# Kernel tuning notes

Hardware: AMD Instinct MI355X
Metric: run time of the kernel (lower is better)

## Reference

```python
import jax, jax.numpy as jnp
import numpy as np

B, L, NE, DOUT = 4, 4096, 64, 64
DI = 128          # backbone model dim (hardcoded d_inner in MambaDoc)
NL = 2            # num_layers
H = 2             # num_heads
N = 128           # state_dim
G = 1             # num_groups
CONV = 4          # conv_size
DIN = 2 * DI      # expand=2 -> 256 inner channels of the mixer
P = DIN // H      # headdim = 128
CCH = DIN + 2 * G * N      # 512 conv channels (x, B, C)
DPROJ = 2 * DIN + 2 * G * N + H  # 770 in_proj output width


def setup_inputs() -> dict:
    key = jax.random.key(0)
    ks = jax.random.split(key, 8)
    s = lambda k, shape, sc: (jax.random.normal(k, shape, jnp.float32) * sc)
    return {
        "x": s(ks[0], (B, L, NE), 1.0),
        "in_w": s(ks[1], (DI, NE), (1.0 / NE) ** 0.5),
        "in_b": jnp.zeros((DI,), jnp.float32),
        "out_w": s(ks[2], (DOUT, DI), (1.0 / DI) ** 0.5),
        "out_b": jnp.zeros((DOUT,), jnp.float32),
        "l_rms_w": jnp.ones((NL, DI), jnp.float32),
        "l_in_w": s(ks[3], (NL, DPROJ, DI), (1.0 / DI) ** 0.5),
        "conv_w": s(ks[4], (NL, CCH, CONV), (1.0 / CONV) ** 0.5),
        "conv_b": jnp.zeros((NL, CCH), jnp.float32),
        "dt_bias": s(ks[5], (NL, H), 0.1),
        "A_log": jnp.zeros((NL, H), jnp.float32),   # A = -exp(A_log) = -1
        "D_p": jnp.ones((NL, H), jnp.float32),
        "gnorm_w": jnp.ones((NL, DIN), jnp.float32),
        "l_out_w": s(ks[6], (NL, DI, DIN), (1.0 / DIN) ** 0.5),
        "fnorm_w": jnp.ones((DI,), jnp.float32),
    }


def _rms(x, w, eps=1e-5):
    return x * jax.lax.rsqrt(jnp.mean(x * x, -1, keepdims=True) + eps) * w


def _mamba_layer(x, rms_w, in_w, cw, cb, dtb, a_log, d, gnw, ow):
    # x: (B,L,DI)
    h = _rms(x, rms_w)
    zxbcdt = jnp.einsum("bld,ed->ble", h, in_w)  # (B,L,770)
    z, xBC, dt = jnp.split(zxbcdt, [DIN, DIN + CCH], axis=-1)
    # causal depthwise conv over time, conv_size taps
    xp = jnp.pad(xBC, ((0, 0), (CONV - 1, 0), (0, 0)))
    xc = cb + sum(xp[:, k:k + L, :] * cw[:, k] for k in range(CONV))
    xc = jax.nn.silu(xc)
    xs, Bm, Cm = jnp.split(xc, [DIN, DIN + G * N], axis=-1)
    xs = xs.reshape(B, L, H, P)
    dt = jax.nn.softplus(dt + dtb)                 # (B,L,H)
    dA = jnp.exp(dt * (-jnp.exp(a_log)))           # (B,L,H) discrete decay

    def step(hc, inp):
        dA_t, dt_t, x_t, B_t, C_t = inp  # (B,H),(B,H),(B,H,P),(B,N),(B,N)
        hc = hc * dA_t[:, :, None, None] + (dt_t[:, :, None] * x_t)[..., None] * B_t[:, None, None, :]
        y = jnp.einsum("bhpn,bn->bhp", hc, C_t)
        return hc, y

    h0 = jnp.zeros((B, H, P, N), x.dtype)
    seq = (jnp.moveaxis(dA, 1, 0), jnp.moveaxis(dt, 1, 0), jnp.moveaxis(xs, 1, 0),
           jnp.moveaxis(Bm, 1, 0), jnp.moveaxis(Cm, 1, 0))
    _, ys = jax.lax.scan(step, h0, seq)
    y = jnp.moveaxis(ys, 0, 1)                     # (B,L,H,P)
    y = y + xs * d[None, None, :, None]            # D skip connection
    y = _rms(y.reshape(B, L, DIN) * jax.nn.silu(z), gnw)  # gated RMSNorm
    return x + jnp.einsum("ble,de->bld", y, ow)


def reference(x, in_w, in_b, out_w, out_b, l_rms_w, l_in_w, conv_w, conv_b,
              dt_bias, A_log, D_p, gnorm_w, l_out_w, fnorm_w):
    xp = jnp.einsum("bln,dn->bld", x, in_w) + in_b
    h = xp
    for i in range(NL):
        h = _mamba_layer(h, l_rms_w[i], l_in_w[i], conv_w[i], conv_b[i],
                         dt_bias[i], A_log[i], D_p[i], gnorm_w[i], l_out_w[i])
    h = _rms(h, fnorm_w)            # backbone final norm
    out = xp + h                    # outer residual in MambaDoc.forward
    return jnp.einsum("bld,od->blo", out, out_w) + out_b
```

## Files before the change

kernel.cpp:

```cpp
#include <hip/hip_runtime.h>
#include <cstddef>
#include <cstdint>


#define LSEQ 4096
#define MTOK 16384

typedef unsigned short u16;
typedef _Float16 f16x8 __attribute__((ext_vector_type(8)));
typedef float f32x4 __attribute__((ext_vector_type(4)));

__device__ __forceinline__ u16 f2h(float x) {
    return __builtin_bit_cast(u16, (_Float16)x);
}
__device__ __forceinline__ float h2f(u16 u) {
    return (float)__builtin_bit_cast(_Float16, u);
}
__device__ __forceinline__ float silu_f(float x) { return x / (1.f + __expf(-x)); }

__device__ __forceinline__ void async_lds16(const void* g, void* l) {
    __builtin_amdgcn_global_load_lds(
        (const __attribute__((address_space(1))) unsigned int*)g,
        (__attribute__((address_space(3))) unsigned int*)l, 16, 0, 0);
}

__device__ __forceinline__ uint4 cvt8(const float* __restrict__ src) {
    float4 a = *(const float4*)src;
    float4 b = *(const float4*)(src + 4);
    union { u16 u[8]; uint4 q; } pk;
    pk.u[0] = f2h(a.x); pk.u[1] = f2h(a.y); pk.u[2] = f2h(a.z); pk.u[3] = f2h(a.w);
    pk.u[4] = f2h(b.x); pk.u[5] = f2h(b.y); pk.u[6] = f2h(b.z); pk.u[7] = f2h(b.w);
    return pk.q;
}

__device__ __forceinline__ uint4 cvt8g(const float* __restrict__ src,
                                       const float* __restrict__ gw) {
    float4 a = *(const float4*)src;
    float4 b = *(const float4*)(src + 4);
    float4 ga = *(const float4*)gw;
    float4 gb = *(const float4*)(gw + 4);
    union { u16 u[8]; uint4 q; } pk;
    pk.u[0] = f2h(a.x * ga.x); pk.u[1] = f2h(a.y * ga.y);
    pk.u[2] = f2h(a.z * ga.z); pk.u[3] = f2h(a.w * ga.w);
    pk.u[4] = f2h(b.x * gb.x); pk.u[5] = f2h(b.y * gb.y);
    pk.u[6] = f2h(b.z * gb.z); pk.u[7] = f2h(b.w * gb.w);
    return pk.q;
}

__global__ __launch_bounds__(256) void gemm_rms0_kernel(
    const float* __restrict__ xf, const float* __restrict__ wf,
    const float* __restrict__ bias, const float* __restrict__ rmsw,
    u16* __restrict__ xp16, u16* __restrict__ hbuf16, u16* __restrict__ hn16)
{
    __shared__ u16 sA[64 * 64];
    __shared__ u16 sW[128 * 64];
    __shared__ float red[64][33];
    __shared__ float srstd[64];
    const int m0 = blockIdx.y * 64;
    const int tid = threadIdx.x, wid = tid >> 6, lane = tid & 63;
    const int wm = (wid >> 1) * 32, wn = (wid & 1) * 64;
    const int quad = lane >> 4, cl = lane & 15;
    #pragma unroll
    for (int i = 0; i < 2; i++) {
        int ck = i * 256 + tid;
        int r = ck >> 3, cc = ck & 7;
        int csw = (cc ^ (r & 7)) << 3;
        *(uint4*)&sA[ck * 8] = cvt8(xf + (size_t)(m0 + r) * 64 + csw);
    }
    #pragma unroll
    for (int i = 0; i < 4; i++) {
        int ck = i * 256 + tid;
        int r = ck >> 3, cc = ck & 7;
        int csw = (cc ^ (r & 7)) << 3;
        *(uint4*)&sW[ck * 8] = cvt8(wf + (size_t)r * 64 + csw);
    }
    __syncthreads();
    f32x4 acc[2][4];
    #pragma unroll
    for (int i = 0; i < 2; i++)
        #pragma unroll
        for (int j = 0; j < 4; j++) acc[i][j] = f32x4{0.f, 0.f, 0.f, 0.f};
    #pragma unroll
    for (int ks = 0; ks < 2; ks++) {
        f16x8 af[2], wv[4];
        int kc = ks * 4 + quad;
        #pragma unroll
        for (int i = 0; i < 2; i++) {
            int r = wm + i * 16 + cl;
            af[i] = *(const f16x8*)&sA[r * 64 + ((kc ^ (r & 7)) << 3)];
        }
        #pragma unroll
        for (int j = 0; j < 4; j++) {
            int r = wn + j * 16 + cl;
            wv[j] = *(const f16x8*)&sW[r * 64 + ((kc ^ (r & 7)) << 3)];
        }
        #pragma unroll
        for (int i = 0; i < 2; i++)
            #pragma unroll
            for (int j = 0; j < 4; j++)
                acc[i][j] = __builtin_amdgcn_mfma_f32_16x16x32_f16(
                    af[i], wv[j], acc[i][j], 0, 0, 0);
    }
    const int slot = (wid & 1) * 16 + cl;
    #pragma unroll
    for (int i = 0; i < 2; i++)
        #pragma unroll
        for (int r = 0; r < 4; r++) {
            int t = wm + i * 16 + quad * 4 + r;
            float ssp = 0.f;
            #pragma unroll
            for (int j = 0; j < 4; j++) {
                int n = wn + j * 16 + cl;
                float v = acc[i][j][r] + bias[n];
                acc[i][j][r] = v;
                ssp += v * v;
            }
            red[t][slot] = ssp;
        }
    __syncthreads();
    if (tid < 64) {
        float s = 0.f;
        #pragma unroll
        for (int sl = 0; sl < 32; sl++) s += red[tid][sl];
        srstd[tid] = rsqrtf(s * (1.f / 128.f) + 1e-5f);
    }
    __syncthreads();
    #pragma unroll
    for (int i = 0; i < 2; i++)
        #pragma unroll
        for (int r = 0; r < 4; r++) {
            int t = wm + i * 16 + quad * 4 + r;
            size_t ob = (size_t)(m0 + t) * 128;
            float rstd = srstd[t];
            #pragma unroll
            for (int j = 0; j < 4; j++) {
                int n = wn + j * 16 + cl;
                float v = acc[i][j][r];
                u16 vh = f2h(v);
                xp16[ob + n] = vh;
                hbuf16[ob + n] = vh;
                hn16[ob + n] = f2h(v * rstd * rmsw[n]);
            }
        }
}

__global__ __launch_bounds__(256) void gemm_inproj_kernel(
    const u16* __restrict__ A, const float* __restrict__ Wf,
    u16* __restrict__ zx16, float* __restrict__ dtb, float* __restrict__ Sb,
    const float* __restrict__ dt_bias, const float* __restrict__ A_log)
{
    __shared__ u16 sA[128 * 64];
    __shared__ u16 sW[128 * 64];
    __shared__ float sdt[2][128];
    const int K = 128, N = 770;
    const int n0 = blockIdx.x * 128, m0 = blockIdx.y * 128;
    const int tid = threadIdx.x, wid = tid >> 6, lane = tid & 63;
    const int wm = (wid >> 1) * 64, wn = (wid & 1) * 64;
    const int quad = lane >> 4, cl = lane & 15;
    f32x4 acc[4][4];
    #pragma unroll
    for (int i = 0; i < 4; i++)
        #pragma unroll
        for (int j = 0; j < 4; j++) acc[i][j] = f32x4{0.f, 0.f, 0.f, 0.f};

    for (int k0 = 0; k0 < K; k0 += 64) {
        #pragma unroll
        for (int i = 0; i < 4; i++) {
            int ck = i * 256 + tid;
            int r = ck >> 3, cc = ck & 7;
            int csw = (cc ^ (r & 7)) << 3;
            async_lds16(A + (size_t)(m0 + r) * K + k0 + csw,
                        (void*)(sA + (i * 256 + (tid & ~63)) * 8));
        }
        #pragma unroll
        for (int i = 0; i < 4; i++) {
            int ck = i * 256 + tid;
            int r = ck >> 3, cc = ck & 7;
            int csw = (cc ^ (r & 7)) << 3;
            int rr = n0 + r; if (rr >= N) rr = N - 1;
            *(uint4*)&sW[ck * 8] = cvt8(Wf + (size_t)rr * K + k0 + csw);
        }
        __syncthreads();
        #pragma unroll
        for (int ks = 0; ks < 2; ks++) {
            f16x8 af[4], wv[4];
            int kc = ks * 4 + quad;
            #pragma unroll
            for (int i = 0; i < 4; i++) {
                int r = wm + i * 16 + cl;
                af[i] = *(const f16x8*)&sA[r * 64 + ((kc ^ (r & 7)) << 3)];
            }
            #pragma unroll
            for (int j = 0; j < 4; j++) {
                int r = wn + j * 16 + cl;
                wv[j] = *(const f16x8*)&sW[r * 64 + ((kc ^ (r & 7)) << 3)];
            }
            #pragma unroll
            for (int i = 0; i < 4; i++)
                #pragma unroll
                for (int j = 0; j < 4; j++)
                    acc[i][j] = __builtin_amdgcn_mfma_f32_16x16x32_f16(
                        af[i], wv[j], acc[i][j], 0, 0, 0);
        }
        __syncthreads();
    }
    if (blockIdx.x < 6) {
        #pragma unroll
        for (int i = 0; i < 4; i++) {
            int m = m0 + wm + i * 16 + quad * 4;
            #pragma unroll
            for (int j = 0; j < 4; j++) {
                int n = n0 + wn + j * 16 + cl;
                #pragma unroll
                for (int r = 0; r < 4; r++)
                    zx16[(size_t)(m + r) * 768 + n] = f2h(acc[i][j][r]);
            }
        }
    } else {
        if ((wid & 1) == 0 && cl < 2) {
            #pragma unroll
            for (int i = 0; i < 4; i++)
                #pragma unroll
                for (int r = 0; r < 4; r++)
                    sdt[cl][wm + i * 16 + quad * 4 + r] = acc[i][0][r];
        }
        __syncthreads();
        const int hh = tid >> 7, t = tid & 127;
        float raw = sdt[hh][t] + dt_bias[hh];
        float dt = fmaxf(raw, 0.f) + log1pf(__expf(-fabsf(raw)));
        dtb[(size_t)(m0 + t) * 2 + hh] = dt;
        float ad = -__expf(A_log[hh]) * dt;
        __syncthreads();
        sdt[hh][t] = ad;
        __syncthreads();
        for (int off = 1; off < 128; off <<= 1) {
            float add = (t >= off) ? sdt[hh][t - off] : 0.f;
            __syncthreads();
            sdt[hh][t] += add;
            __syncthreads();
        }
        Sb[(size_t)(m0 + t) * 2 + hh] = sdt[hh][t];
    }
}

__global__ __launch_bounds__(512) void chunkstate_conv_kernel(
    const u16* __restrict__ zx16, const float* __restrict__ cw,
    const float* __restrict__ cb, const float* __restrict__ dtb,
    const float* __restrict__ Sb, u16* __restrict__ Hb)
{
    __shared__ u16 raw[2560 * 8];
    __shared__ u16 XT[128 * 128];
    __shared__ u16 BT[128 * 128];
    __shared__ float scw[2][128][4];
    __shared__ float scb[2][128];
    __shared__ float ssw[128];
    const int c = blockIdx.x, h = blockIdx.y, b = blockIdx.z;
    const int tid = threadIdx.x, wid = tid >> 6, lane = tid & 63;
    const int quad = lane >> 4, cl = lane & 15;
    const int tok0 = b * LSEQ + c * 128;
    for (int idx = tid; idx < 256; idx += 512) {
        int grp = idx >> 7, j = idx & 127;
        int ch = grp ? (256 + j) : (128 * h + j);
        float4 w4 = *(const float4*)&cw[ch * 4];
        scw[grp][j][0] = w4.x; scw[grp][j][1] = w4.y;
        scw[grp][j][2] = w4.z; scw[grp][j][3] = w4.w;
        scb[grp][j] = cb[ch];
    }
    if (tid < 128) {
        float Sl = Sb[(size_t)(tok0 + 127) * 2 + h];
        ssw[tid] = __expf(Sl - Sb[(size_t)(tok0 + tid) * 2 + h])
                   * dtb[(size_t)(tok0 + tid) * 2 + h];
    }
    #pragma unroll
    for (int i = 0; i < 5; i++) {
        int ck = i * 512 + tid;
        int r = ck >> 4; if (r > 130) r = 130;
        int cc = ck & 15;
        int tok = tok0 - 3 + r; if (tok < 0) tok = 0;
        async_lds16(zx16 + (size_t)tok * 768 + 256 + 128 * h + ((cc ^ (r & 15)) << 3),
                    (void*)(raw + (i * 512 + (tid & ~63)) * 8));
    }
    __syncthreads();
    if (c == 0 && tid < 48) *(uint4*)&raw[tid * 8] = make_uint4(0, 0, 0, 0);
    __syncthreads();
    #pragma unroll
    for (int it = 0; it < 4; it++) {
        int idx = it * 512 + tid;
        int s = idx & 127, pg = idx >> 7;
        f16x8 v[4];
        #pragma unroll
        for (int k = 0; k < 4; k++) {
            int rr = s + k;
            v[k] = *(const f16x8*)&raw[rr * 128 + ((pg ^ (rr & 15)) << 3)];
        }
        #pragma unroll
        for (int j = 0; j < 8; j++) {
            int p = pg * 8 + j;
            float o = scb[0][p] + (float)v[0][j] * scw[0][p][0]
                    + (float)v[1][j] * scw[0][p][1]
                    + (float)v[2][j] * scw[0][p][2]
                    + (float)v[3][j] * scw[0][p][3];
            o = silu_f(o);
            XT[p * 128 + (((s >> 3) ^ (p & 15)) << 3) + (s & 7)] = f2h(o);
        }
    }
    __syncthreads();
    #pragma unroll
    for (int i = 0; i < 5; i++) {
        int ck = i * 512 + tid;
        int r = ck >> 4; if (r > 130) r = 130;
        int cc = ck & 15;
        int tok = tok0 - 3 + r; if (tok < 0) tok = 0;
        async_lds16(zx16 + (size_t)tok * 768 + 512 + ((cc ^ (r & 15)) << 3),
                    (void*)(raw + (i * 512 + (tid & ~63)) * 8));
    }
    __syncthreads();
    if (c == 0 && tid < 48) *(uint4*)&raw[tid * 8] = make_uint4(0, 0, 0, 0);
    __syncthreads();
    #pragma unroll
    for (int it = 0; it < 4; it++) {
        int idx = it * 512 + tid;
        int s = idx & 127, ng = idx >> 7;
        f16x8 v[4];
        #pragma unroll
        for (int k = 0; k < 4; k++) {
            int rr = s + k;
            v[k] = *(const f16x8*)&raw[rr * 128 + ((ng ^ (rr & 15)) << 3)];
        }
        float wsv = ssw[s];
        #pragma unroll
        for (int j = 0; j < 8; j++) {
            int n = ng * 8 + j;
            float o = scb[1][n] + (float)v[0][j] * scw[1][n][0]
                    + (float)v[1][j] * scw[1][n][1]
                    + (float)v[2][j] * scw[1][n][2]
                    + (float)v[3][j] * scw[1][n][3];
            o = silu_f(o) * wsv;
            BT[n * 128 + (((s >> 3) ^ (n & 15)) << 3) + (s & 7)] = f2h(o);
        }
    }
    __syncthreads();
    const size_t blk = ((size_t)((b * 2 + h) * 32 + c)) << 14;
    const int wm = (wid >> 1) * 32, wn = (wid & 1) * 64;
    f32x4 acc[2][4];
    #pragma unroll
    for (int i = 0; i < 2; i++)
        #pragma unroll
        for (int j = 0; j < 4; j++) acc[i][j] = f32x4{0.f, 0.f, 0.f, 0.f};
    #pragma unroll
    for (int ks = 0; ks < 4; ks++) {
        f16x8 xa[2], bb[4];
        int kc = ks * 4 + quad;
        #pragma unroll
        for (int i = 0; i < 2; i++) {
            int r = wm + i * 16 + cl;
            xa[i] = *(const f16x8*)&XT[r * 128 + ((kc ^ (r & 15)) << 3)];
        }
        #pragma unroll
        for (int j = 0; j < 4; j++) {
            int r = wn + j * 16 + cl;
            bb[j] = *(const f16x8*)&BT[r * 128 + ((kc ^ (r & 15)) << 3)];
        }
        #pragma unroll
        for (int i = 0; i < 2; i++)
            #pragma unroll
            for (int j = 0; j < 4; j++)
                acc[i][j] = __builtin_amdgcn_mfma_f32_16x16x32_f16(
                    xa[i], bb[j], acc[i][j], 0, 0, 0);
    }
    u16* out = Hb + blk;
    #pragma unroll
    for (int i = 0; i < 2; i++)
        #pragma unroll
        for (int j = 0; j < 4; j++)
            #pragma unroll
            for (int r = 0; r < 4; r++)
                out[(size_t)(wm + i * 16 + quad * 4 + r) * 128 + wn + j * 16 + cl]
                    = f2h(acc[i][j][r]);
}

__global__ __launch_bounds__(256) void statecombine_kernel(
    const float* __restrict__ Sb, const u16* __restrict__ Hb,
    u16* __restrict__ Hbf)
{
    const int e = blockIdx.x * 256 + threadIdx.x;
    const int h = blockIdx.y, b = blockIdx.z;
    const size_t base = ((size_t)((b * 2 + h) * 32)) << 14;
    float state = 0.f;
    for (int c = 0; c < 32; c++) {
        size_t idx = base + ((size_t)c << 14) + e;
        float v = h2f(Hb[idx]);
        Hbf[idx] = f2h(state);
        float dec = __expf(Sb[(size_t)(b * LSEQ + c * 128 + 127) * 2 + h]);
        state = dec * state + v;
    }
}

__global__ __launch_bounds__(512) void ssd_ph_kernel(
    const u16* __restrict__ zx16, const u16* __restrict__ Hbf,
    const float* __restrict__ dtb, const float* __restrict__ Sb,
    const float* __restrict__ cw, const float* __restrict__ cb,
    const float* __restrict__ Dp, u16* __restrict__ g16)
{
    __shared__ u16 raw[2560 * 8];
    __shared__ u16 XT[128 * 128];
    __shared__ u16 Btok[128 * 128];
    __shared__ u16 Ctok[128 * 128];
    __shared__ float sS[128], sdt[128];
    __shared__ float scw[3][128][4];
    __shared__ float scb[3][128];
    const int c = blockIdx.x, h = blockIdx.y, b = blockIdx.z;
    const int tid = threadIdx.x, wid = tid >> 6, lane = tid & 63;
    const int quad = lane >> 4, cl = lane & 15;
    const int tok0 = b * LSEQ + c * 128;
    const size_t blk = ((size_t)((b * 2 + h) * 32 + c)) << 14;
    for (int idx = tid; idx < 384; idx += 512) {
        int grp = idx >> 7, j = idx & 127;
        int ch = (grp == 0) ? (128 * h + j) : (grp == 1 ? 256 + j : 384 + j);
        float4 w4 = *(const float4*)&cw[ch * 4];
        scw[grp][j][0] = w4.x; scw[grp][j][1] = w4.y;
        scw[grp][j][2] = w4.z; scw[grp][j][3] = w4.w;
        scb[grp][j] = cb[ch];
    }
    if (tid < 128) {
        sS[tid] = Sb[(size_t)(tok0 + tid) * 2 + h];
        sdt[tid] = dtb[(size_t)(tok0 + tid) * 2 + h];
    }
    #pragma unroll
    for (int i = 0; i < 5; i++) {
        int ck = i * 512 + tid;
        int r = ck >> 4; if (r > 130) r = 130;
        int cc = ck & 15;
        int tok = tok0 - 3 + r; if (tok < 0) tok = 0;
        async_lds16(zx16 + (size_t)tok * 768 + 256 + 128 * h + ((cc ^ (r & 15)) << 3),
                    (void*)(raw + (i * 512 + (tid & ~63)) * 8));
    }
    __syncthreads();
    if (c == 0 && tid < 48) *(uint4*)&raw[tid * 8] = make_uint4(0, 0, 0, 0);
    __syncthreads();
    #pragma unroll
    for (int it = 0; it < 4; it++) {
        int idx = it * 512 + tid;
        int s = idx & 127, pg = idx >> 7;
        f16x8 v[4];
        #pragma unroll
        for (int k = 0; k < 4; k++) {
            int rr = s + k;
            v[k] = *(const f16x8*)&raw[rr * 128 + ((pg ^ (rr & 15)) << 3)];
        }
        #pragma unroll
        for (int j = 0; j < 8; j++) {
            int p = pg * 8 + j;
            float o = scb[0][p] + (float)v[0][j] * scw[0][p][0]
                    + (float)v[1][j] * scw[0][p][1]
                    + (float)v[2][j] * scw[0][p][2]
                    + (float)v[3][j] * scw[0][p][3];
            XT[p * 128 + (((s >> 3) ^ (p & 15)) << 3) + (s & 7)] = f2h(silu_f(o));
        }
    }
    __syncthreads();
    #pragma unroll
    for (int i = 0; i < 5; i++) {
        int ck = i * 512 + tid;
        int r = ck >> 4; if (r > 130) r = 130;
        int cc = ck & 15;
        int tok = tok0 - 3 + r; if (tok < 0) tok = 0;
        async_lds16(zx16 + (size_t)tok * 768 + 512 + ((cc ^ (r & 15)) << 3),
                    (void*)(raw + (i * 512 + (tid & ~63)) * 8));
    }
    __syncthreads();
    if (c == 0 && tid < 48) *(uint4*)&raw[tid * 8] = make_uint4(0, 0, 0, 0);
    __syncthreads();
    #pragma unroll
    for (int it = 0; it < 4; it++) {
        int idx = it * 512 + tid;
        int t = idx & 127, ng = idx >> 7;
        f16x8 v[4];
        #pragma unroll
        for (int k = 0; k < 4; k++) {
            int rr = t + k;
            v[k] = *(const f16x8*)&raw[rr * 128 + ((ng ^ (rr & 15)) << 3)];
        }
        union { u16 u[8]; uint4 q; } pk;
        #pragma unroll
        for (int j = 0; j < 8; j++) {
            int n = ng * 8 + j;
            float o = scb[1][n] + (float)v[0][j] * scw[1][n][0]
                    + (float)v[1][j] * scw[1][n][1]
                    + (float)v[2][j] * scw[1][n][2]
                    + (float)v[3][j] * scw[1][n][3];
            pk.u[j] = f2h(silu_f(o));
        }
        *(uint4*)&Btok[t * 128 + ((ng ^ (t & 15)) << 3)] = pk.q;
    }
    __syncthreads();
    #pragma unroll
    for (int i = 0; i < 5; i++) {
        int ck = i * 512 + tid;
        int r = ck >> 4; if (r > 130) r = 130;
        int cc = ck & 15;
        int tok = tok0 - 3 + r; if (tok < 0) tok = 0;
        async_lds16(zx16 + (size_t)tok * 768 + 640 + ((cc ^ (r & 15)) << 3),
                    (void*)(raw + (i * 512 + (tid & ~63)) * 8));
    }
    __syncthreads();
    if (c == 0 && tid < 48) *(uint4*)&raw[tid * 8] = make_uint4(0, 0, 0, 0);
    __syncthreads();
    #pragma unroll
    for (int it = 0; it < 4; it++) {
        int idx = it * 512 + tid;
        int t = idx & 127, ng = idx >> 7;
        f16x8 v[4];
        #pragma unroll
        for (int k = 0; k < 4; k++) {
            int rr = t + k;
            v[k] = *(const f16x8*)&raw[rr * 128 + ((ng ^ (rr & 15)) << 3)];
        }
        union { u16 u[8]; uint4 q; } pk;
        #pragma unroll
        for (int j = 0; j < 8; j++) {
            int n = ng * 8 + j;
            float o = scb[2][n] + (float)v[0][j] * scw[2][n][0]
                    + (float)v[1][j] * scw[2][n][1]
                    + (float)v[2][j] * scw[2][n][2]
                    + (float)v[3][j] * scw[2][n][3];
            pk.u[j] = f2h(silu_f(o));
        }
        *(uint4*)&Ctok[t * 128 + ((ng ^ (t & 15)) << 3)] = pk.q;
    }
    __syncthreads();
    #pragma unroll
    for (int i = 0; i < 4; i++) {
        int ck = i * 512 + tid;
        int r = ck >> 4, cc = ck & 15;
        async_lds16(Hbf + blk + (size_t)r * 128 + ((cc ^ (r & 15)) << 3),
                    (void*)(raw + (i * 512 + (tid & ~63)) * 8));
    }
    __syncthreads();
    const int wm = (wid >> 1) * 32, wn = (wid & 1) * 64;
    f32x4 acc[2][4];
    #pragma unroll
    for (int i = 0; i < 2; i++)
        #pragma unroll
        for (int j = 0; j < 4; j++) acc[i][j] = f32x4{0.f, 0.f, 0.f, 0.f};
    #pragma unroll
    for (int ks = 0; ks < 4; ks++) {
        f16x8 ca[2], hb[4];
        int kc = ks * 4 + quad;
        #pragma unroll
        for (int i = 0; i < 2; i++) {
            int r = wm + i * 16 + cl;
            ca[i] = *(const f16x8*)&Ctok[r * 128 + ((kc ^ (r & 15)) << 3)];
        }
        #pragma unroll
        for (int j = 0; j < 4; j++) {
            int r = wn + j * 16 + cl;
            hb[j] = *(const f16x8*)&raw[r * 128 + ((kc ^ (r & 15)) << 3)];
        }
        #pragma unroll
        for (int i = 0; i < 2; i++)
            #pragma unroll
            for (int j = 0; j < 4; j++)
                acc[i][j] = __builtin_amdgcn_mfma_f32_16x16x32_f16(
                    ca[i], hb[j], acc[i][j], 0, 0, 0);
    }
    #pragma unroll
    for (int i = 0; i < 2; i++)
        #pragma unroll
        for (int r = 0; r < 4; r++) {
            float e = __expf(sS[wm + i * 16 + quad * 4 + r]);
            #pragma unroll
            for (int j = 0; j < 4; j++) acc[i][j][r] *= e;
        }
    f32x4 sacc[2][4];
    #pragma unroll
    for (int i = 0; i < 2; i++)
        #pragma unroll
        for (int j = 0; j < 4; j++) sacc[i][j] = f32x4{0.f, 0.f, 0.f, 0.f};
    #pragma unroll
    for (int ks = 0; ks < 4; ks++) {
        f16x8 cs[2], bs[4];
        int kc = ks * 4 + quad;
        #pragma unroll
        for (int i2 = 0; i2 < 2; i2++) {
            int r = wm + i2 * 16 + cl;
            cs[i2] = *(const f16x8*)&Ctok[r * 128 + ((kc ^ (r & 15)) << 3)];
        }
        #pragma unroll
        for (int j = 0; j < 4; j++) {
            int r = wn + j * 16 + cl;
            bs[j] = *(const f16x8*)&Btok[r * 128 + ((kc ^ (r & 15)) << 3)];
        }
        #pragma unroll
        for (int i2 = 0; i2 < 2; i2++)
            #pragma unroll
            for (int j = 0; j < 4; j++)
                if (wm + i2 * 16 + 15 >= wn + j * 16)
                    sacc[i2][j] = __builtin_amdgcn_mfma_f32_16x16x32_f16(
                        cs[i2], bs[j], sacc[i2][j], 0, 0, 0);
    }
    __syncthreads();
    #pragma unroll
    for (int i2 = 0; i2 < 2; i2++)
        #pragma unroll
        for (int r = 0; r < 4; r++) {
            int t = wm + i2 * 16 + quad * 4 + r;
            float Stv = sS[t];
            #pragma unroll
            for (int j = 0; j < 4; j++) {
                int s = wn + j * 16 + cl;
                float gv = 0.f;
                if (s <= t) gv = sacc[i2][j][r] * __expf(Stv - sS[s]) * sdt[s];
                raw[t * 128 + (((s >> 3) ^ (t & 15)) << 3) + (s & 7)] = f2h(gv);
            }
        }
    __syncthreads();
    #pragma unroll
    for (int ks = 0; ks < 4; ks++) {
        f16x8 ga[2], xb[4];
        int kc = ks * 4 + quad;
        #pragma unroll
        for (int i = 0; i < 2; i++) {
            int r = wm + i * 16 + cl;
            ga[i] = *(const f16x8*)&raw[r * 128 + ((kc ^ (r & 15)) << 3)];
        }
        #pragma unroll
        for (int j = 0; j < 4; j++) {
            int r = wn + j * 16 + cl;
            xb[j] = *(const f16x8*)&XT[r * 128 + ((kc ^ (r & 15)) << 3)];
        }
        #pragma unroll
        for (int i = 0; i < 2; i++)
            #pragma unroll
            for (int j = 0; j < 4; j++)
                acc[i][j] = __builtin_amdgcn_mfma_f32_16x16x32_f16(
                    ga[i], xb[j], acc[i][j], 0, 0, 0);
    }
    const float dco = Dp[h];
    #pragma unroll
    for (int i = 0; i < 2; i++)
        #pragma unroll
        for (int r = 0; r < 4; r++) {
            int t = wm + i * 16 + quad * 4 + r;
            u16* row = g16 + (size_t)(tok0 + t) * 256 + h * 128;
            #pragma unroll
            for (int j = 0; j < 4; j++) {
                int p = wn + j * 16 + cl;
                float xv = h2f(XT[p * 128 + (((t >> 3) ^ (p & 15)) << 3) + (t & 7)]);
                float zv = h2f(zx16[(size_t)(tok0 + t) * 768 + h * 128 + p]);
                row[p] = f2h((acc[i][j][r] + dco * xv) * silu_f(zv));
            }
        }
}

__global__ __launch_bounds__(256) void gemm_outrms_kernel(
    const u16* __restrict__ A, const float* __restrict__ Wf,
    const float* __restrict__ gnw, const float* __restrict__ rmsw,
    u16* __restrict__ xp16, u16* __restrict__ hbuf16, u16* __restrict__ hn16,
    const float* __restrict__ out_wf, const float* __restrict__ out_b,
    float* __restrict__ dout, int mode)
{
    __shared__ u16 sA[64 * 64];
    __shared__ u16 sW[128 * 64];
    __shared__ float red[64][33];
    __shared__ float srstd[64];
    __shared__ float redp[64][5];
    __shared__ float rstdg[64];
    __shared__ u16 hn2[64 * 128];
    __shared__ u16 ow[64 * 128];
    const int K = 256;
    const int m0 = blockIdx.y * 64;
    const int tid = threadIdx.x, wid = tid >> 6, lane = tid & 63;
    const int wm = (wid >> 1) * 32, wn = (wid & 1) * 64;
    const int quad = lane >> 4, cl = lane & 15;
    {
        int t = tid >> 2, q = tid & 3;
        const u16* row = A + (size_t)(m0 + t) * 256 + q * 64;
        float ss = 0.f;
        #pragma unroll
        for (int u = 0; u < 8; u++) {
            f16x8 v = *(const f16x8*)&row[u * 8];
            #pragma unroll
            for (int j = 0; j < 8; j++) { float f = (float)v[j]; ss += f * f; }
        }
        redp[t][q] = ss;
    }
    __syncthreads();
    if (tid < 64)
        rstdg[tid] = rsqrtf((redp[tid][0] + redp[tid][1] + redp[tid][2]
                             + redp[tid][3]) * (1.f / 256.f) + 1e-5f);
    f32x4 acc[2][4];
    #pragma unroll
    for (int i = 0; i < 2; i++)
        #pragma unroll
        for (int j = 0; j < 4; j++) acc[i][j] = f32x4{0.f, 0.f, 0.f, 0.f};

    for (int k0 = 0; k0 < K; k0 += 64) {
        #pragma unroll
        for (int i = 0; i < 2; i++) {
            int ck = i * 256 + tid;
            int r = ck >> 3, cc = ck & 7;
            int csw = (cc ^ (r & 7)) << 3;
            async_lds16(A + (size_t)(m0 + r) * K + k0 + csw,
                        (void*)(sA + (i * 256 + (tid & ~63)) * 8));
        }
        #pragma unroll
        for (int i = 0; i < 4; i++) {
            int ck = i * 256 + tid;
            int r = ck >> 3, cc = ck & 7;
            int csw = (cc ^ (r & 7)) << 3;
            *(uint4*)&sW[ck * 8] = cvt8g(Wf + (size_t)r * K + k0 + csw,
                                         gnw + k0 + csw);
        }
        __syncthreads();
        #pragma unroll
        for (int ks = 0; ks < 2; ks++) {
            f16x8 af[2], wv[4];
            int kc = ks * 4 + quad;
            #pragma unroll
            for (int i = 0; i < 2; i++) {
                int r = wm + i * 16 + cl;
                af[i] = *(const f16x8*)&sA[r * 64 + ((kc ^ (r & 7)) << 3)];
            }
            #pragma unroll
            for (int j = 0; j < 4; j++) {
                int r = wn + j * 16 + cl;
                wv[j] = *(const f16x8*)&sW[r * 64 + ((kc ^ (r & 7)) << 3)];
            }
            #pragma unroll
            for (int i = 0; i < 2; i++)
                #pragma unroll
                for (int j = 0; j < 4; j++)
                    acc[i][j] = __builtin_amdgcn_mfma_f32_16x16x32_f16(
                        af[i], wv[j], acc[i][j], 0, 0, 0);
        }
        __syncthreads();
    }
    const int slot = (wid & 1) * 16 + cl;
    #pragma unroll
    for (int i = 0; i < 2; i++)
        #pragma unroll
        for (int r = 0; r < 4; r++) {
            int t = wm + i * 16 + quad * 4 + r;
            size_t ob = (size_t)(m0 + t) * 128;
            float rg = rstdg[t];
            float ssp = 0.f;
            #pragma unroll
            for (int j = 0; j < 4; j++) {
                int n = wn + j * 16 + cl;
                float v = acc[i][j][r] * rg + h2f(hbuf16[ob + n]);
                acc[i][j][r] = v;
                ssp += v * v;
            }
            red[t][slot] = ssp;
        }
    __syncthreads();
    if (tid < 64) {
        float s = 0.f;
        #pragma unroll
        for (int sl = 0; sl < 32; sl++) s += red[tid][sl];
        srstd[tid] = rsqrtf(s * (1.f / 128.f) + 1e-5f);
    }
    __syncthreads();
    #pragma unroll
    for (int i = 0; i < 2; i++)
        #pragma unroll
        for (int r = 0; r < 4; r++) {
            int t = wm + i * 16 + quad * 4 + r;
            size_t ob = (size_t)(m0 + t) * 128;
            float rstd = srstd[t];
            #pragma unroll
            for (int j = 0; j < 4; j++) {
                int n = wn + j * 16 + cl;
                float v = acc[i][j][r];
                float val = v * rstd * rmsw[n];
                if (mode == 1) {
                    hbuf16[ob + n] = f2h(v);
                    hn16[ob + n] = f2h(val);
                } else {
                    val += h2f(xp16[ob + n]);
                    hn2[t * 128 + (((n >> 3) ^ (t & 15)) << 3) + (n & 7)] = f2h(val);
                }
            }
        }
    if (mode == 1) return;
    #pragma unroll
    for (int i = 0; i < 4; i++) {
        int ck = i * 256 + tid;
        int rr = ck >> 4, cc = ck & 15;
        int csw = (cc ^ (rr & 15)) << 3;
        *(uint4*)&ow[ck * 8] = cvt8(out_wf + (size_t)rr * 128 + csw);
    }
    __syncthreads();
    const int wm4 = (wid >> 1) * 32, wn4 = (wid & 1) * 32;
    f32x4 acc2[2][2];
    #pragma unroll
    for (int i = 0; i < 2; i++)
        #pragma unroll
        for (int j = 0; j < 2; j++) acc2[i][j] = f32x4{0.f, 0.f, 0.f, 0.f};
    #pragma unroll
    for (int ks = 0; ks < 4; ks++) {
        f16x8 af2[2], wf2[2];
        int kc = ks * 4 + quad;
        #pragma unroll
        for (int i = 0; i < 2; i++) {
            int r = wm4 + i * 16 + cl;
            af2[i] = *(const f16x8*)&hn2[r * 128 + ((kc ^ (r & 15)) << 3)];
        }
        #pragma unroll
        for (int j = 0; j < 2; j++) {
            int rr = wn4 + j * 16 + cl;
            wf2[j] = *(const f16x8*)&ow[rr * 128 + ((kc ^ (rr & 15)) << 3)];
        }
        #pragma unroll
        for (int i = 0; i < 2; i++)
            #pragma unroll
            for (int j = 0; j < 2; j++)
                acc2[i][j] = __builtin_amdgcn_mfma_f32_16x16x32_f16(
                    af2[i], wf2[j], acc2[i][j], 0, 0, 0);
    }
    #pragma unroll
    for (int i = 0; i < 2; i++) {
        int m = m0 + wm4 + i * 16 + quad * 4;
        #pragma unroll
        for (int j = 0; j < 2; j++) {
            int n = wn4 + j * 16 + cl;
            float bv = out_b[n];
            #pragma unroll
            for (int r = 0; r < 4; r++)
                dout[(size_t)(m + r) * 64 + n] = acc2[i][j][r] + bv;
        }
    }
}

extern "C" void kernel_launch(void* const* d_in, const int* in_sizes, int n_in,
                              void* d_out, int out_size, void* d_ws, size_t ws_size,
                              hipStream_t stream)
{
    (void)in_sizes; (void)n_in; (void)out_size; (void)ws_size;
    const float* x       = (const float*)d_in[0];
    const float* in_w    = (const float*)d_in[1];
    const float* in_b    = (const float*)d_in[2];
    const float* out_w   = (const float*)d_in[3];
    const float* out_b   = (const float*)d_in[4];
    const float* l_rms_w = (const float*)d_in[5];
    const float* l_in_w  = (const float*)d_in[6];
    const float* conv_w  = (const float*)d_in[7];
    const float* conv_b  = (const float*)d_in[8];
    const float* dt_bias = (const float*)d_in[9];
    const float* A_log   = (const float*)d_in[10];
    const float* D_p     = (const float*)d_in[11];
    const float* gnorm_w = (const float*)d_in[12];
    const float* l_out_w = (const float*)d_in[13];
    const float* fnorm_w = (const float*)d_in[14];

    char* w = (char*)d_ws;
    u16*   xp16   = (u16*)(w);
    u16*   hbuf16 = (u16*)(w + 4194304);
    u16*   hn16   = (u16*)(w + 8388608);
    u16*   zx16   = (u16*)(w + 12582912);
    float* dtb    = (float*)(w + 37748736);
    float* Sb     = (float*)(w + 37879808);
    u16*   Hb     = (u16*)(w + 38010880);
    u16*   Hbf    = (u16*)(w + 46399488);
    u16*   g16    = (u16*)(w + 54788096);

    gemm_rms0_kernel<<<dim3(1, 256), 256, 0, stream>>>(
        x, in_w, in_b, l_rms_w, xp16, hbuf16, hn16);

    for (int i = 0; i < 2; i++) {
        gemm_inproj_kernel<<<dim3(7, 128), 256, 0, stream>>>(
            hn16, l_in_w + (size_t)i * 770 * 128, zx16, dtb, Sb,
            dt_bias + i * 2, A_log + i * 2);
        chunkstate_conv_kernel<<<dim3(32, 2, 4), 512, 0, stream>>>(
            zx16, conv_w + i * 2048, conv_b + i * 512, dtb, Sb, Hb);
        statecombine_kernel<<<dim3(64, 2, 4), 256, 0, stream>>>(Sb, Hb, Hbf);
        ssd_ph_kernel<<<dim3(32, 2, 4), 512, 0, stream>>>(
            zx16, Hbf, dtb, Sb, conv_w + i * 2048, conv_b + i * 512,
            D_p + i * 2, g16);
        gemm_outrms_kernel<<<dim3(1, 256), 256, 0, stream>>>(
            g16, l_out_w + (size_t)i * 128 * 256, gnorm_w + i * 256,
            (i == 0) ? (l_rms_w + 128) : fnorm_w, xp16, hbuf16, hn16,
            out_w, out_b, (float*)d_out, (i == 0) ? 1 : 3);
    }
}
```

Baseline: 231.4 us.

## Fuse chunk-state, state-combine and SSD kernels into one persistent kernel with grid barriers

Merges the three per-layer SSD kernels into a single 256-block kernel. Blocks sync through atomic-counter grid barriers between computing chunk states, scanning them across chunks, and producing outputs. The conv/silu of x and B is now computed once instead of being repeated in two kernels, and two launches per layer go away. The cost is spin-wait barriers, which assume all 256 blocks are co-resident (512 threads and large LDS per block), plus a memset of the counters.

```diff
diff --git a/kernel.cpp b/kernel.cpp
--- a/kernel.cpp
+++ b/kernel.cpp
@@ -45,6 +45,18 @@
     pk.u[4] = f2h(b.x * gb.x); pk.u[5] = f2h(b.y * gb.y);
     pk.u[6] = f2h(b.z * gb.z); pk.u[7] = f2h(b.w * gb.w);
     return pk.q;
+}
+
+__device__ __forceinline__ void grid_barrier(unsigned int* cnt, unsigned int target) {
+    __syncthreads();
+    if (threadIdx.x == 0) {
+        __threadfence();
+        atomicAdd(cnt, 1u);
+        while (atomicAdd(cnt, 0u) < target)
+            __builtin_amdgcn_s_sleep(8);
+        __threadfence();
+    }
+    __syncthreads();
 }
 
 __global__ __launch_bounds__(256) void gemm_rms0_kernel(
@@ -243,170 +255,18 @@
     }
 }
 
-__global__ __launch_bounds__(512) void chunkstate_conv_kernel(
-    const u16* __restrict__ zx16, const float* __restrict__ cw,
-    const float* __restrict__ cb, const float* __restrict__ dtb,
-    const float* __restrict__ Sb, u16* __restrict__ Hb)
+__global__ __launch_bounds__(512) void layer_ssd_kernel(
+    const u16* __restrict__ zx16, const float* __restrict__ dtb,
+    const float* __restrict__ Sb, const float* __restrict__ cw,
+    const float* __restrict__ cb, const float* __restrict__ Dp,
+    u16* __restrict__ Hb, u16* __restrict__ Hbf, u16* __restrict__ g16,
+    unsigned int* __restrict__ cnt)
 {
     __shared__ u16 raw[2560 * 8];
     __shared__ u16 XT[128 * 128];
-    __shared__ u16 BT[128 * 128];
-    __shared__ float scw[2][128][4];
-    __shared__ float scb[2][128];
-    __shared__ float ssw[128];
-    const int c = blockIdx.x, h = blockIdx.y, b = blockIdx.z;
-    const int tid = threadIdx.x, wid = tid >> 6, lane = tid & 63;
-    const int quad = lane >> 4, cl = lane & 15;
-    const int tok0 = b * LSEQ + c * 128;
-    for (int idx = tid; idx < 256; idx += 512) {
-        int grp = idx >> 7, j = idx & 127;
-        int ch = grp ? (256 + j) : (128 * h + j);
-        float4 w4 = *(const float4*)&cw[ch * 4];
-        scw[grp][j][0] = w4.x; scw[grp][j][1] = w4.y;
-        scw[grp][j][2] = w4.z; scw[grp][j][3] = w4.w;
-        scb[grp][j] = cb[ch];
-    }
-    if (tid < 128) {
-        float Sl = Sb[(size_t)(tok0 + 127) * 2 + h];
-        ssw[tid] = __expf(Sl - Sb[(size_t)(tok0 + tid) * 2 + h])
-                   * dtb[(size_t)(tok0 + tid) * 2 + h];
-    }
-    #pragma unroll
-    for (int i = 0; i < 5; i++) {
-        int ck = i * 512 + tid;
-        int r = ck >> 4; if (r > 130) r = 130;
-        int cc = ck & 15;
-        int tok = tok0 - 3 + r; if (tok < 0) tok = 0;
-        async_lds16(zx16 + (size_t)tok * 768 + 256 + 128 * h + ((cc ^ (r & 15)) << 3),
-                    (void*)(raw + (i * 512 + (tid & ~63)) * 8));
-    }
-    __syncthreads();
-    if (c == 0 && tid < 48) *(uint4*)&raw[tid * 8] = make_uint4(0, 0, 0, 0);
-    __syncthreads();
-    #pragma unroll
-    for (int it = 0; it < 4; it++) {
-        int idx = it * 512 + tid;
-        int s = idx & 127, pg = idx >> 7;
-        f16x8 v[4];
-        #pragma unroll
-        for (int k = 0; k < 4; k++) {
-            int rr = s + k;
-            v[k] = *(const f16x8*)&raw[rr * 128 + ((pg ^ (rr & 15)) << 3)];
-        }
-        #pragma unroll
-        for (int j = 0; j < 8; j++) {
-            int p = pg * 8 + j;
-            float o = scb[0][p] + (float)v[0][j] * scw[0][p][0]
-                    + (float)v[1][j] * scw[0][p][1]
-                    + (float)v[2][j] * scw[0][p][2]
-                    + (float)v[3][j] * scw[0][p][3];
-            o = silu_f(o);
-            XT[p * 128 + (((s >> 3) ^ (p & 15)) << 3) + (s & 7)] = f2h(o);
-        }
-    }
-    __syncthreads();
-    #pragma unroll
-    for (int i = 0; i < 5; i++) {
-        int ck = i * 512 + tid;
-        int r = ck >> 4; if (r > 130) r = 130;
-        int cc = ck & 15;
-        int tok = tok0 - 3 + r; if (tok < 0) tok = 0;
-        async_lds16(zx16 + (size_t)tok * 768 + 512 + ((cc ^ (r & 15)) << 3),
-                    (void*)(raw + (i * 512 + (tid & ~63)) * 8));
-    }
-    __syncthreads();
-    if (c == 0 && tid < 48) *(uint4*)&raw[tid * 8] = make_uint4(0, 0, 0, 0);
-    __syncthreads();
-    #pragma unroll
-    for (int it = 0; it < 4; it++) {
-        int idx = it * 512 + tid;
-        int s = idx & 127, ng = idx >> 7;
-        f16x8 v[4];
-        #pragma unroll
-        for (int k = 0; k < 4; k++) {
-            int rr = s + k;
-            v[k] = *(const f16x8*)&raw[rr * 128 + ((ng ^ (rr & 15)) << 3)];
-        }
-        float wsv = ssw[s];
-        #pragma unroll
-        for (int j = 0; j < 8; j++) {
-            int n = ng * 8 + j;
-            float o = scb[1][n] + (float)v[0][j] * scw[1][n][0]
-                    + (float)v[1][j] * scw[1][n][1]
-                    + (float)v[2][j] * scw[1][n][2]
-                    + (float)v[3][j] * scw[1][n][3];
-            o = silu_f(o) * wsv;
-            BT[n * 128 + (((s >> 3) ^ (n & 15)) << 3) + (s & 7)] = f2h(o);
-        }
-    }
-    __syncthreads();
-    const size_t blk = ((size_t)((b * 2 + h) * 32 + c)) << 14;
-    const int wm = (wid >> 1) * 32, wn = (wid & 1) * 64;
-    f32x4 acc[2][4];
-    #pragma unroll
-    for (int i = 0; i < 2; i++)
-        #pragma unroll
-        for (int j = 0; j < 4; j++) acc[i][j] = f32x4{0.f, 0.f, 0.f, 0.f};
-    #pragma unroll
-    for (int ks = 0; ks < 4; ks++) {
-        f16x8 xa[2], bb[4];
-        int kc = ks * 4 + quad;
-        #pragma unroll
-        for (int i = 0; i < 2; i++) {
-            int r = wm + i * 16 + cl;
-            xa[i] = *(const f16x8*)&XT[r * 128 + ((kc ^ (r & 15)) << 3)];
-        }
-        #pragma unroll
-        for (int j = 0; j < 4; j++) {
-            int r = wn + j * 16 + cl;
-            bb[j] = *(const f16x8*)&BT[r * 128 + ((kc ^ (r & 15)) << 3)];
-        }
-        #pragma unroll
-        for (int i = 0; i < 2; i++)
-            #pragma unroll
-            for (int j = 0; j < 4; j++)
-                acc[i][j] = __builtin_amdgcn_mfma_f32_16x16x32_f16(
-                    xa[i], bb[j], acc[i][j], 0, 0, 0);
-    }
-    u16* out = Hb + blk;
-    #pragma unroll
-    for (int i = 0; i < 2; i++)
-        #pragma unroll
-        for (int j = 0; j < 4; j++)
-            #pragma unroll
-            for (int r = 0; r < 4; r++)
-                out[(size_t)(wm + i * 16 + quad * 4 + r) * 128 + wn + j * 16 + cl]
-                    = f2h(acc[i][j][r]);
-}
-
-__global__ __launch_bounds__(256) void statecombine_kernel(
-    const float* __restrict__ Sb, const u16* __restrict__ Hb,
-    u16* __restrict__ Hbf)
-{
-    const int e = blockIdx.x * 256 + threadIdx.x;
-    const int h = blockIdx.y, b = blockIdx.z;
-    const size_t base = ((size_t)((b * 2 + h) * 32)) << 14;
-    float state = 0.f;
-    for (int c = 0; c < 32; c++) {
-        size_t idx = base + ((size_t)c << 14) + e;
-        float v = h2f(Hb[idx]);
-        Hbf[idx] = f2h(state);
-        float dec = __expf(Sb[(size_t)(b * LSEQ + c * 128 + 127) * 2 + h]);
-        state = dec * state + v;
-    }
-}
-
-__global__ __launch_bounds__(512) void ssd_ph_kernel(
-    const u16* __restrict__ zx16, const u16* __restrict__ Hbf,
-    const float* __restrict__ dtb, const float* __restrict__ Sb,
-    const float* __restrict__ cw, const float* __restrict__ cb,
-    const float* __restrict__ Dp, u16* __restrict__ g16)
-{
-    __shared__ u16 raw[2560 * 8];
-    __shared__ u16 XT[128 * 128];
+    __shared__ u16 slotA[128 * 128];
     __shared__ u16 Btok[128 * 128];
-    __shared__ u16 Ctok[128 * 128];
-    __shared__ float sS[128], sdt[128];
+    __shared__ float sS[128], sdt[128], ssw[128];
     __shared__ float scw[3][128][4];
     __shared__ float scb[3][128];
     const int c = blockIdx.x, h = blockIdx.y, b = blockIdx.z;
@@ -423,8 +283,12 @@
         scb[grp][j] = cb[ch];
     }
     if (tid < 128) {
-        sS[tid] = Sb[(size_t)(tok0 + tid) * 2 + h];
-        sdt[tid] = dtb[(size_t)(tok0 + tid) * 2 + h];
+        float Sv = Sb[(size_t)(tok0 + tid) * 2 + h];
+        float dv = dtb[(size_t)(tok0 + tid) * 2 + h];
+        sS[tid] = Sv;
+        sdt[tid] = dv;
+        float Sl = Sb[(size_t)(tok0 + 127) * 2 + h];
+        ssw[tid] = __expf(Sl - Sv) * dv;
     }
     #pragma unroll
     for (int i = 0; i < 5; i++) {
@@ -474,13 +338,14 @@
     #pragma unroll
     for (int it = 0; it < 4; it++) {
         int idx = it * 512 + tid;
-        int t = idx & 127, ng = idx >> 7;
+        int s = idx & 127, ng = idx >> 7;
         f16x8 v[4];
         #pragma unroll
         for (int k = 0; k < 4; k++) {
-            int rr = t + k;
+            int rr = s + k;
             v[k] = *(const f16x8*)&raw[rr * 128 + ((ng ^ (rr & 15)) << 3)];
         }
+        float wsv = ssw[s];
         union { u16 u[8]; uint4 q; } pk;
         #pragma unroll
         for (int j = 0; j < 8; j++) {
@@ -489,11 +354,68 @@
                     + (float)v[1][j] * scw[1][n][1]
                     + (float)v[2][j] * scw[1][n][2]
                     + (float)v[3][j] * scw[1][n][3];
-            pk.u[j] = f2h(silu_f(o));
-        }
-        *(uint4*)&Btok[t * 128 + ((ng ^ (t & 15)) << 3)] = pk.q;
-    }
-    __syncthreads();
+            o = silu_f(o);
+            pk.u[j] = f2h(o);
+            slotA[n * 128 + (((s >> 3) ^ (n & 15)) << 3) + (s & 7)] = f2h(o * wsv);
+        }
+        *(uint4*)&Btok[s * 128 + ((ng ^ (s & 15)) << 3)] = pk.q;
+    }
+    __syncthreads();
+    {
+        const int wm = (wid >> 1) * 32, wn = (wid & 1) * 64;
+        f32x4 acc[2][4];
+        #pragma unroll
+        for (int i = 0; i < 2; i++)
+            #pragma unroll
+            for (int j = 0; j < 4; j++) acc[i][j] = f32x4{0.f, 0.f, 0.f, 0.f};
+        #pragma unroll
+        for (int ks = 0; ks < 4; ks++) {
+            f16x8 xa[2], bb[4];
+            int kc = ks * 4 + quad;
+            #pragma unroll
+            for (int i = 0; i < 2; i++) {
+                int r = wm + i * 16 + cl;
+                xa[i] = *(const f16x8*)&XT[r * 128 + ((kc ^ (r & 15)) << 3)];
+            }
+            #pragma unroll
+            for (int j = 0; j < 4; j++) {
+                int r = wn + j * 16 + cl;
+                bb[j] = *(const f16x8*)&slotA[r * 128 + ((kc ^ (r & 15)) << 3)];
+            }
+            #pragma unroll
+            for (int i = 0; i < 2; i++)
+                #pragma unroll
+                for (int j = 0; j < 4; j++)
+                    acc[i][j] = __builtin_amdgcn_mfma_f32_16x16x32_f16(
+                        xa[i], bb[j], acc[i][j], 0, 0, 0);
+        }
+        u16* out = Hb + blk;
+        #pragma unroll
+        for (int i = 0; i < 2; i++)
+            #pragma unroll
+            for (int j = 0; j < 4; j++)
+                #pragma unroll
+                for (int r = 0; r < 4; r++)
+                    out[(size_t)(wm + i * 16 + quad * 4 + r) * 128 + wn + j * 16 + cl]
+                        = f2h(acc[i][j][r]);
+    }
+    grid_barrier(cnt, 256);
+    {
+        int gblk = (b * 2 + h) * 32 + c;
+        int seq = gblk >> 5;
+        int e = (gblk & 31) * 512 + tid;
+        size_t base = (size_t)seq << 19;
+        int sb_ = seq >> 1, sh_ = seq & 1;
+        float state = 0.f;
+        for (int c2 = 0; c2 < 32; c2++) {
+            size_t idx = base + ((size_t)c2 << 14) + e;
+            float v = h2f(Hb[idx]);
+            Hbf[idx] = f2h(state);
+            float dec = __expf(Sb[(size_t)(sb_ * LSEQ + c2 * 128 + 127) * 2 + sh_]);
+            state = dec * state + v;
+        }
+    }
+    grid_barrier(cnt, 512);
     #pragma unroll
     for (int i = 0; i < 5; i++) {
         int ck = i * 512 + tid;
@@ -526,7 +448,7 @@
                     + (float)v[3][j] * scw[2][n][3];
             pk.u[j] = f2h(silu_f(o));
         }
-        *(uint4*)&Ctok[t * 128 + ((ng ^ (t & 15)) << 3)] = pk.q;
+        *(uint4*)&slotA[t * 128 + ((ng ^ (t & 15)) << 3)] = pk.q;
     }
     __syncthreads();
     #pragma unroll
@@ -550,7 +472,7 @@
         #pragma unroll
         for (int i = 0; i < 2; i++) {
             int r = wm + i * 16 + cl;
-            ca[i] = *(const f16x8*)&Ctok[r * 128 + ((kc ^ (r & 15)) << 3)];
+            ca[i] = *(const f16x8*)&slotA[r * 128 + ((kc ^ (r & 15)) << 3)];
         }
         #pragma unroll
         for (int j = 0; j < 4; j++) {
@@ -584,7 +506,7 @@
         #pragma unroll
         for (int i2 = 0; i2 < 2; i2++) {
             int r = wm + i2 * 16 + cl;
-            cs[i2] = *(const f16x8*)&Ctok[r * 128 + ((kc ^ (r & 15)) << 3)];
+            cs[i2] = *(const f16x8*)&slotA[r * 128 + ((kc ^ (r & 15)) << 3)];
         }
         #pragma unroll
         for (int j = 0; j < 4; j++) {
@@ -864,6 +786,9 @@
     u16*   Hb     = (u16*)(w + 38010880);
     u16*   Hbf    = (u16*)(w + 46399488);
     u16*   g16    = (u16*)(w + 54788096);
+    unsigned int* cnt = (unsigned int*)(w + 63176704);
+
+    hipMemsetAsync(cnt, 0, 8, stream);
 
     gemm_rms0_kernel<<<dim3(1, 256), 256, 0, stream>>>(
         x, in_w, in_b, l_rms_w, xp16, hbuf16, hn16);
@@ -872,12 +797,9 @@
         gemm_inproj_kernel<<<dim3(7, 128), 256, 0, stream>>>(
             hn16, l_in_w + (size_t)i * 770 * 128, zx16, dtb, Sb,
             dt_bias + i * 2, A_log + i * 2);
-        chunkstate_conv_kernel<<<dim3(32, 2, 4), 512, 0, stream>>>(
-            zx16, conv_w + i * 2048, conv_b + i * 512, dtb, Sb, Hb);
-        statecombine_kernel<<<dim3(64, 2, 4), 256, 0, stream>>>(Sb, Hb, Hbf);
-        ssd_ph_kernel<<<dim3(32, 2, 4), 512, 0, stream>>>(
-            zx16, Hbf, dtb, Sb, conv_w + i * 2048, conv_b + i * 512,
-            D_p + i * 2, g16);
+        layer_ssd_kernel<<<dim3(32, 2, 4), 512, 0, stream>>>(
+            zx16, dtb, Sb, conv_w + i * 2048, conv_b + i * 512,
+            D_p + i * 2, Hb, Hbf, g16, cnt + i);
         gemm_outrms_kernel<<<dim3(1, 256), 256, 0, stream>>>(
             g16, l_out_w + (size_t)i * 128 * 256, gnorm_w + i * 256,
             (i == 0) ? (l_rms_w + 128) : fnorm_w, xp16, hbuf16, hn16,
```

Result: slower. 300.2 us (+29.7%).
